# Performance work log

Measured on AMD Instinct MI355X. Metric: run time of the kernel, lower is better.

## Reference

```python
import jax, jax.numpy as jnp
import numpy as np

B, H, W, C = 8, 64, 64, 256
CK = C // 8  # key/query dim of conv_f / conv_g


def setup_inputs() -> dict:
    key = jax.random.key(0)
    ks = jax.random.split(key, 10)
    s = lambda fan_in: 1.0 / np.sqrt(fan_in)
    return {
        "x": jax.random.normal(ks[0], (B, H, W, C), dtype=jnp.float32),
        "Wf": jax.random.normal(ks[1], (C, CK), dtype=jnp.float32) * s(C),
        "bf": jnp.zeros((CK,), dtype=jnp.float32),
        "Wg": jax.random.normal(ks[2], (C, CK), dtype=jnp.float32) * s(C),
        "bg": jnp.zeros((CK,), dtype=jnp.float32),
        "Wh": jax.random.normal(ks[3], (C, C), dtype=jnp.float32) * s(C),
        "bh": jnp.zeros((C,), dtype=jnp.float32),
        "Wo": jax.random.normal(ks[4], (C, C), dtype=jnp.float32) * s(C),
        "bo": jnp.zeros((C,), dtype=jnp.float32),
        # original init is zeros; use a random scalar so output/grads are nontrivial
        "gamma": jax.random.normal(ks[5], (1,), dtype=jnp.float32),
    }


def reference(x, Wf, bf, Wg, bg, Wh, bh, Wo, bo, gamma):
    b, h, w, c = x.shape
    n = h * w
    xf = x.reshape(b, n, c)                       # flatten spatial: [B, N, C]
    # 1x1 convs == per-pixel matmuls
    f = xf @ Wf + bf                              # [B, N, C//8]
    g = xf @ Wg + bg                              # [B, N, C//8]
    hh = xf @ Wh + bh                             # [B, N, C]
    # scores[b, i, j] = <g_i, f_j>; softmax over j (keys)
    scores = jnp.einsum("bnd,bmd->bnm", g, f)     # [B, N, N]
    attn = jax.nn.softmax(scores, axis=-1)
    o = jnp.einsum("bnm,bmc->bnc", attn, hh)      # [B, N, C]
    o = o @ Wo + bo                               # conv_o (1x1)
    out = gamma * o + xf                          # gamma residual
    return out.reshape(b, h, w, c)
```

## Files before the change

kernel.cpp:

```cpp
#include <hip/hip_runtime.h>
#include <hip/hip_fp16.h>
#include <hip/hip_bf16.h>

constexpr int BB  = 8;
constexpr int NN  = 4096;
constexpr int CC  = 256;
constexpr int CKK = 32;

typedef __attribute__((ext_vector_type(8))) short    short8;
typedef __attribute__((ext_vector_type(8))) _Float16 half8;
typedef __attribute__((ext_vector_type(4))) _Float16 half4;
typedef __attribute__((ext_vector_type(4))) float    f32x4;

__device__ __forceinline__ unsigned short bf16_bits(float v) {
    __hip_bfloat16 h = __float2bfloat16(v);
    return *reinterpret_cast<unsigned short*>(&h);
}
__device__ __forceinline__ float bf16_val(unsigned short u) {
    __hip_bfloat16 h = *reinterpret_cast<__hip_bfloat16*>(&u);
    return __bfloat162float(h);
}

__global__ __launch_bounds__(256) void prep_kernel(
    const float* __restrict__ Wf, const float* __restrict__ Wg,
    const float* __restrict__ Wh, const float* __restrict__ Wo,
    unsigned short* __restrict__ WThi, unsigned short* __restrict__ WTlo)
{
    const int n = blockIdx.x;
    const int k = threadIdx.x;
    float v;
    if      (n < 256) v = Wh[k * 256 + n];
    else if (n < 288) v = Wf[k * 32 + (n - 256)];
    else if (n < 320) v = Wg[k * 32 + (n - 288)];
    else              v = Wo[k * 256 + (n - 320)];
    const unsigned short hi = bf16_bits(v);
    WThi[n * 256 + k] = hi;
    WTlo[n * 256 + k] = bf16_bits(v - bf16_val(hi));
}

__global__ __launch_bounds__(256) void fgh_kernel(
    const float* __restrict__ x,
    const unsigned short* __restrict__ WThi, const unsigned short* __restrict__ WTlo,
    const float* __restrict__ bf, const float* __restrict__ bg,
    const float* __restrict__ bh,
    _Float16* __restrict__ fbuf, _Float16* __restrict__ gbuf,
    _Float16* __restrict__ hhT)
{
    const int tid = threadIdx.x, w = tid >> 6, lane = tid & 63;
    const int ln = lane & 15, lq = lane >> 4;
    const int px0 = blockIdx.x * 256 + w * 64;
    const int n0  = blockIdx.y * 64;

    f32x4 acc[4][4];
    #pragma unroll
    for (int i = 0; i < 4; ++i)
        #pragma unroll
        for (int j = 0; j < 4; ++j) acc[i][j] = {0.f, 0.f, 0.f, 0.f};

    #pragma unroll 1
    for (int kc = 0; kc < 8; ++kc) {
        const int k0 = kc * 32;
        short8 Ahi[4], Alo[4];
        #pragma unroll
        for (int mt = 0; mt < 4; ++mt) {
            float av[8];
            const float* xp = &x[(size_t)(px0 + mt * 16 + ln) * CC + k0 + lq * 8];
            *(float4*)&av[0] = *(const float4*)xp;
            *(float4*)&av[4] = *(const float4*)(xp + 4);
            #pragma unroll
            for (int j = 0; j < 8; ++j) {
                const unsigned short h = bf16_bits(av[j]);
                Ahi[mt][j] = (short)h;
                Alo[mt][j] = (short)bf16_bits(av[j] - bf16_val(h));
            }
        }
        #pragma unroll
        for (int nt = 0; nt < 4; ++nt) {
            const size_t boff = (size_t)(n0 + nt * 16 + ln) * 256 + k0 + lq * 8;
            const short8 Bhi = *(const short8*)&WThi[boff];
            const short8 Blo = *(const short8*)&WTlo[boff];
            #pragma unroll
            for (int mt = 0; mt < 4; ++mt) {
                acc[mt][nt] = __builtin_amdgcn_mfma_f32_16x16x32_bf16(Ahi[mt], Bhi, acc[mt][nt], 0, 0, 0);
                acc[mt][nt] = __builtin_amdgcn_mfma_f32_16x16x32_bf16(Ahi[mt], Blo, acc[mt][nt], 0, 0, 0);
                acc[mt][nt] = __builtin_amdgcn_mfma_f32_16x16x32_bf16(Alo[mt], Bhi, acc[mt][nt], 0, 0, 0);
            }
        }
    }

    const int b = px0 >> 12;
    if (blockIdx.y < 4) {
        #pragma unroll
        for (int nt = 0; nt < 4; ++nt) {
            const int c = n0 + nt * 16 + ln;
            const float bias = bh[c];
            #pragma unroll
            for (int mt = 0; mt < 4; ++mt) {
                half4 hv;
                #pragma unroll
                for (int r = 0; r < 4; ++r) hv[r] = (_Float16)(acc[mt][nt][r] + bias);
                const int npix = (px0 & (NN - 1)) + mt * 16 + lq * 4;
                *(half4*)&hhT[((size_t)(b * CC + c)) * NN + npix] = hv;
            }
        }
    } else {
        #pragma unroll
        for (int nt = 0; nt < 4; ++nt) {
            const int d = (nt & 1) * 16 + ln;
            const float bias = (nt < 2) ? bf[d] : bg[d];
            _Float16* dst = (nt < 2) ? fbuf : gbuf;
            #pragma unroll
            for (int mt = 0; mt < 4; ++mt)
                #pragma unroll
                for (int r = 0; r < 4; ++r)
                    dst[(size_t)(px0 + mt * 16 + lq * 4 + r) * CKK + d] =
                        (_Float16)(acc[mt][nt][r] + bias);
        }
    }
}

__global__ __launch_bounds__(256) void attn_kernel(
    const _Float16* __restrict__ fbuf, const _Float16* __restrict__ gbuf,
    const _Float16* __restrict__ hhT, float* __restrict__ obuf)
{
    __shared__ _Float16 P[2][64 * 72];
    __shared__ float mxbuf[4][64];
    __shared__ float rsbuf[4][64];

    const int tid = threadIdx.x, w = tid >> 6, lane = tid & 63;
    const int ln = lane & 15, lq = lane >> 4;
    const int b  = blockIdx.x & 7;
    const int q0 = (blockIdx.x >> 3) * 64;
    const int cb = w * 64;

    const f32x4 zero = {0.f, 0.f, 0.f, 0.f};
    constexpr float LOG2E = 1.4426950408889634f;

    half8 Bg[4];
    #pragma unroll
    for (int qt = 0; qt < 4; ++qt)
        Bg[qt] = *(const half8*)&gbuf[(size_t)(b * NN + q0 + qt * 16 + ln) * CKK + lq * 8];

    float mx[4];
    #pragma unroll
    for (int qt = 0; qt < 4; ++qt) mx[qt] = -1e30f;
    #pragma unroll 1
    for (int j0 = 0; j0 < NN; j0 += 64) {
        const half8 Af = *(const half8*)
            &fbuf[(size_t)(b * NN + j0 + w * 16 + ln) * CKK + lq * 8];
        #pragma unroll
        for (int qt = 0; qt < 4; ++qt) {
            const f32x4 s = __builtin_amdgcn_mfma_f32_16x16x32_f16(Af, Bg[qt], zero, 0, 0, 0);
            mx[qt] = fmaxf(mx[qt], fmaxf(fmaxf(s[0], s[1]), fmaxf(s[2], s[3])));
        }
    }
    #pragma unroll
    for (int qt = 0; qt < 4; ++qt) {
        mx[qt] = fmaxf(mx[qt], __shfl_xor(mx[qt], 16));
        mx[qt] = fmaxf(mx[qt], __shfl_xor(mx[qt], 32));
    }
    if (lane < 16) {
        #pragma unroll
        for (int qt = 0; qt < 4; ++qt) mxbuf[w][qt * 16 + ln] = mx[qt];
    }
    __syncthreads();
    float mk[4];
    #pragma unroll
    for (int qt = 0; qt < 4; ++qt)
        mk[qt] = LOG2E * fmaxf(fmaxf(mxbuf[0][qt * 16 + ln], mxbuf[1][qt * 16 + ln]),
                               fmaxf(mxbuf[2][qt * 16 + ln], mxbuf[3][qt * 16 + ln]));

    f32x4 O[4][4];
    #pragma unroll
    for (int qt = 0; qt < 4; ++qt)
        #pragma unroll
        for (int ct = 0; ct < 4; ++ct) O[qt][ct] = zero;
    float psum[4] = {0.f, 0.f, 0.f, 0.f};

    #pragma unroll 1
    for (int j0 = 0; j0 < NN; j0 += 64) {
        const int buf = (j0 >> 6) & 1;

        half8 Bh[4][2];
        #pragma unroll
        for (int ct = 0; ct < 4; ++ct)
            #pragma unroll
            for (int kh = 0; kh < 2; ++kh)
                Bh[ct][kh] = *(const half8*)
                    &hhT[((size_t)(b * CC + cb + ct * 16 + ln)) * NN + j0 + kh * 32 + lq * 8];

        const half8 Af = *(const half8*)
            &fbuf[(size_t)(b * NN + j0 + w * 16 + ln) * CKK + lq * 8];
        #pragma unroll
        for (int qt = 0; qt < 4; ++qt) {
            const f32x4 s = __builtin_amdgcn_mfma_f32_16x16x32_f16(Af, Bg[qt], zero, 0, 0, 0);
            half4 ph;
            float ps = 0.f;
            #pragma unroll
            for (int r = 0; r < 4; ++r) {
                const float p = exp2f(fmaf(s[r], LOG2E, -mk[qt]));
                ps += p;
                ph[r] = (_Float16)p;
            }
            psum[qt] += ps;
            *(half4*)&P[buf][(qt * 16 + ln) * 72 + w * 16 + lq * 4] = ph;
        }
        __syncthreads();

        #pragma unroll
        for (int qt = 0; qt < 4; ++qt) {
            const half8 Ap0 = *(const half8*)&P[buf][(qt * 16 + ln) * 72 + lq * 8];
            const half8 Ap1 = *(const half8*)&P[buf][(qt * 16 + ln) * 72 + 32 + lq * 8];
            #pragma unroll
            for (int ct = 0; ct < 4; ++ct) {
                O[qt][ct] = __builtin_amdgcn_mfma_f32_16x16x32_f16(Ap0, Bh[ct][0], O[qt][ct], 0, 0, 0);
                O[qt][ct] = __builtin_amdgcn_mfma_f32_16x16x32_f16(Ap1, Bh[ct][1], O[qt][ct], 0, 0, 0);
            }
        }
    }

    #pragma unroll
    for (int qt = 0; qt < 4; ++qt) {
        psum[qt] += __shfl_xor(psum[qt], 16);
        psum[qt] += __shfl_xor(psum[qt], 32);
    }
    if (lane < 16) {
        #pragma unroll
        for (int qt = 0; qt < 4; ++qt) rsbuf[w][qt * 16 + ln] = psum[qt];
    }
    __syncthreads();

    #pragma unroll
    for (int qt = 0; qt < 4; ++qt)
        #pragma unroll
        for (int r = 0; r < 4; ++r) {
            const int q = qt * 16 + lq * 4 + r;
            const float rinv = 1.0f / (rsbuf[0][q] + rsbuf[1][q] + rsbuf[2][q] + rsbuf[3][q]);
            #pragma unroll
            for (int ct = 0; ct < 4; ++ct)
                obuf[((size_t)(b * NN + q0 + q)) * CC + cb + ct * 16 + ln] = O[qt][ct][r] * rinv;
        }
}

__global__ __launch_bounds__(256) void out_kernel(
    const float* __restrict__ obuf,
    const unsigned short* __restrict__ WThi, const unsigned short* __restrict__ WTlo,
    const float* __restrict__ bo, const float* __restrict__ gamma,
    const float* __restrict__ x, float* __restrict__ out)
{
    const int tid = threadIdx.x, w = tid >> 6, lane = tid & 63;
    const int ln = lane & 15, lq = lane >> 4;
    const int px0 = blockIdx.x * 256 + w * 64;
    const int n0  = blockIdx.y * 64;

    f32x4 acc[4][4];
    #pragma unroll
    for (int i = 0; i < 4; ++i)
        #pragma unroll
        for (int j = 0; j < 4; ++j) acc[i][j] = {0.f, 0.f, 0.f, 0.f};

    #pragma unroll 1
    for (int kc = 0; kc < 8; ++kc) {
        const int k0 = kc * 32;
        short8 Ahi[4], Alo[4];
        #pragma unroll
        for (int mt = 0; mt < 4; ++mt) {
            float av[8];
            const float* op = &obuf[(size_t)(px0 + mt * 16 + ln) * CC + k0 + lq * 8];
            *(float4*)&av[0] = *(const float4*)op;
            *(float4*)&av[4] = *(const float4*)(op + 4);
            #pragma unroll
            for (int j = 0; j < 8; ++j) {
                const unsigned short h = bf16_bits(av[j]);
                Ahi[mt][j] = (short)h;
                Alo[mt][j] = (short)bf16_bits(av[j] - bf16_val(h));
            }
        }
        #pragma unroll
        for (int nt = 0; nt < 4; ++nt) {
            const size_t boff = (size_t)(320 + n0 + nt * 16 + ln) * 256 + k0 + lq * 8;
            const short8 Bhi = *(const short8*)&WThi[boff];
            const short8 Blo = *(const short8*)&WTlo[boff];
            #pragma unroll
            for (int mt = 0; mt < 4; ++mt) {
                acc[mt][nt] = __builtin_amdgcn_mfma_f32_16x16x32_bf16(Ahi[mt], Bhi, acc[mt][nt], 0, 0, 0);
                acc[mt][nt] = __builtin_amdgcn_mfma_f32_16x16x32_bf16(Ahi[mt], Blo, acc[mt][nt], 0, 0, 0);
                acc[mt][nt] = __builtin_amdgcn_mfma_f32_16x16x32_bf16(Alo[mt], Bhi, acc[mt][nt], 0, 0, 0);
            }
        }
    }

    const float gm = gamma[0];
    #pragma unroll
    for (int nt = 0; nt < 4; ++nt) {
        const int c = n0 + nt * 16 + ln;
        const float bias = bo[c];
        #pragma unroll
        for (int mt = 0; mt < 4; ++mt)
            #pragma unroll
            for (int r = 0; r < 4; ++r) {
                const size_t idx = (size_t)(px0 + mt * 16 + lq * 4 + r) * CC + c;
                out[idx] = gm * (acc[mt][nt][r] + bias) + x[idx];
            }
    }
}

extern "C" void kernel_launch(void* const* d_in, const int* in_sizes, int n_in,
                              void* d_out, int out_size, void* d_ws, size_t ws_size,
                              hipStream_t stream)
{
    (void)in_sizes; (void)n_in; (void)out_size; (void)ws_size;

    const float* x     = (const float*)d_in[0];
    const float* Wf    = (const float*)d_in[1];
    const float* bf    = (const float*)d_in[2];
    const float* Wg    = (const float*)d_in[3];
    const float* bg    = (const float*)d_in[4];
    const float* Wh    = (const float*)d_in[5];
    const float* bh    = (const float*)d_in[6];
    const float* Wo    = (const float*)d_in[7];
    const float* bo    = (const float*)d_in[8];
    const float* gamma = (const float*)d_in[9];
    float* out = (float*)d_out;

    _Float16* fbuf = (_Float16*)d_ws;
    _Float16* gbuf = fbuf + (size_t)BB * NN * CKK;
    _Float16* hhT  = gbuf + (size_t)BB * NN * CKK;
    float*    obuf = (float*)(hhT + (size_t)BB * CC * NN);
    unsigned short* WThi = (unsigned short*)(obuf + (size_t)BB * NN * CC);
    unsigned short* WTlo = WThi + (size_t)576 * 256;

    prep_kernel<<<576, 256, 0, stream>>>(Wf, Wg, Wh, Wo, WThi, WTlo);
    fgh_kernel<<<dim3(BB * NN / 256, 5), 256, 0, stream>>>(x, WThi, WTlo, bf, bg, bh,
                                                           fbuf, gbuf, hhT);
    attn_kernel<<<BB * NN / 64, 256, 0, stream>>>(fbuf, gbuf, hhT, obuf);
    out_kernel<<<dim3(BB * NN / 256, 4), 256, 0, stream>>>(obuf, WThi, WTlo, bo, gamma, x, out);
}
```

Baseline: 331.7 us.

## Software-pipeline attention loop with double-buffered hh loads and MFMA priority

Restructures the attention main loop to unroll by two with register double-buffering of the hh tiles and f fragments, so the global loads for the next 64-key block are issued before the current block's P·V MFMAs. It also prefetches the f fragment in the max pass, raises wave priority around the MFMA phase, and asks for two blocks per CU via launch bounds. The aim is to hide global-memory latency behind compute. The cost is higher register pressure from the duplicated Bh buffers, which could cause spills under the occupancy target.

```diff
diff --git a/kernel.cpp b/kernel.cpp
--- a/kernel.cpp
+++ b/kernel.cpp
@@ -119,7 +119,7 @@
     }
 }
 
-__global__ __launch_bounds__(256) void attn_kernel(
+__global__ __launch_bounds__(256, 2) void attn_kernel(
     const _Float16* __restrict__ fbuf, const _Float16* __restrict__ gbuf,
     const _Float16* __restrict__ hhT, float* __restrict__ obuf)
 {
@@ -141,18 +141,23 @@
     for (int qt = 0; qt < 4; ++qt)
         Bg[qt] = *(const half8*)&gbuf[(size_t)(b * NN + q0 + qt * 16 + ln) * CKK + lq * 8];
 
+    const _Float16* fb = &fbuf[(size_t)(b * NN + w * 16 + ln) * CKK + lq * 8];
+    const _Float16* hb = &hhT[((size_t)(b * CC + cb + ln)) * NN + lq * 8];
+
     float mx[4];
     #pragma unroll
     for (int qt = 0; qt < 4; ++qt) mx[qt] = -1e30f;
+    half8 Afc = *(const half8*)fb;
     #pragma unroll 1
     for (int j0 = 0; j0 < NN; j0 += 64) {
-        const half8 Af = *(const half8*)
-            &fbuf[(size_t)(b * NN + j0 + w * 16 + ln) * CKK + lq * 8];
+        const int jn = (j0 + 64 < NN) ? j0 + 64 : j0;
+        const half8 Afn = *(const half8*)&fb[(size_t)jn * CKK];
         #pragma unroll
         for (int qt = 0; qt < 4; ++qt) {
-            const f32x4 s = __builtin_amdgcn_mfma_f32_16x16x32_f16(Af, Bg[qt], zero, 0, 0, 0);
+            const f32x4 s = __builtin_amdgcn_mfma_f32_16x16x32_f16(Afc, Bg[qt], zero, 0, 0, 0);
             mx[qt] = fmaxf(mx[qt], fmaxf(fmaxf(s[0], s[1]), fmaxf(s[2], s[3])));
         }
+        Afc = Afn;
     }
     #pragma unroll
     for (int qt = 0; qt < 4; ++qt) {
@@ -177,20 +182,7 @@
         for (int ct = 0; ct < 4; ++ct) O[qt][ct] = zero;
     float psum[4] = {0.f, 0.f, 0.f, 0.f};
 
-    #pragma unroll 1
-    for (int j0 = 0; j0 < NN; j0 += 64) {
-        const int buf = (j0 >> 6) & 1;
-
-        half8 Bh[4][2];
-        #pragma unroll
-        for (int ct = 0; ct < 4; ++ct)
-            #pragma unroll
-            for (int kh = 0; kh < 2; ++kh)
-                Bh[ct][kh] = *(const half8*)
-                    &hhT[((size_t)(b * CC + cb + ct * 16 + ln)) * NN + j0 + kh * 32 + lq * 8];
-
-        const half8 Af = *(const half8*)
-            &fbuf[(size_t)(b * NN + j0 + w * 16 + ln) * CKK + lq * 8];
+    auto phaseA = [&](const half8& Af, _Float16* Pb) {
         #pragma unroll
         for (int qt = 0; qt < 4; ++qt) {
             const f32x4 s = __builtin_amdgcn_mfma_f32_16x16x32_f16(Af, Bg[qt], zero, 0, 0, 0);
@@ -203,20 +195,52 @@
                 ph[r] = (_Float16)p;
             }
             psum[qt] += ps;
-            *(half4*)&P[buf][(qt * 16 + ln) * 72 + w * 16 + lq * 4] = ph;
-        }
-        __syncthreads();
-
+            *(half4*)&Pb[(qt * 16 + ln) * 72 + w * 16 + lq * 4] = ph;
+        }
+    };
+
+    auto loadBh = [&](half8 (&Bh)[4][2], int j0) {
+        #pragma unroll
+        for (int ct = 0; ct < 4; ++ct)
+            #pragma unroll
+            for (int kh = 0; kh < 2; ++kh)
+                Bh[ct][kh] = *(const half8*)&hb[(size_t)ct * 16 * NN + j0 + kh * 32];
+    };
+
+    auto phaseB = [&](const half8 (&Bh)[4][2], const _Float16* Pb) {
+        __builtin_amdgcn_s_setprio(1);
         #pragma unroll
         for (int qt = 0; qt < 4; ++qt) {
-            const half8 Ap0 = *(const half8*)&P[buf][(qt * 16 + ln) * 72 + lq * 8];
-            const half8 Ap1 = *(const half8*)&P[buf][(qt * 16 + ln) * 72 + 32 + lq * 8];
+            const half8 Ap0 = *(const half8*)&Pb[(qt * 16 + ln) * 72 + lq * 8];
+            const half8 Ap1 = *(const half8*)&Pb[(qt * 16 + ln) * 72 + 32 + lq * 8];
             #pragma unroll
             for (int ct = 0; ct < 4; ++ct) {
                 O[qt][ct] = __builtin_amdgcn_mfma_f32_16x16x32_f16(Ap0, Bh[ct][0], O[qt][ct], 0, 0, 0);
                 O[qt][ct] = __builtin_amdgcn_mfma_f32_16x16x32_f16(Ap1, Bh[ct][1], O[qt][ct], 0, 0, 0);
             }
         }
+        __builtin_amdgcn_s_setprio(0);
+    };
+
+    half8 Bh0[4][2], Bh1[4][2];
+    half8 Af0, Af1;
+    loadBh(Bh0, 0);
+    Af0 = *(const half8*)fb;
+
+    #pragma unroll 1
+    for (int j0 = 0; j0 < NN; j0 += 128) {
+        phaseA(Af0, P[0]);
+        __syncthreads();
+        loadBh(Bh1, j0 + 64);
+        Af1 = *(const half8*)&fb[(size_t)(j0 + 64) * CKK];
+        phaseB(Bh0, P[0]);
+        phaseA(Af1, P[1]);
+        __syncthreads();
+        if (j0 + 128 < NN) {
+            loadBh(Bh0, j0 + 128);
+            Af0 = *(const half8*)&fb[(size_t)(j0 + 128) * CKK];
+        }
+        phaseB(Bh1, P[1]);
     }
 
     #pragma unroll
```

Measured after the change: 328.9 us. Within noise of the previous version (-0.8%).
